# Optimization experiments

Hardware: AMD Instinct MI355X
Metric: run time of the kernel (lower is better)

The kernel has to match this reference:

```python
import jax, jax.numpy as jnp
from jax import lax
import numpy as np

OUT_SCALE = 0.001
DN = ('NCHW', 'OIHW', 'NCHW')


def _dw_res_gelu(v, w, b):
    # depthwise 3x3 conv (groups = C) + bias, residual add, exact GELU (torch nn.GELU default)
    y = lax.conv_general_dilated(v, w, (1, 1), ((1, 1), (1, 1)),
                                 feature_group_count=v.shape[1],
                                 dimension_numbers=DN)
    y = y + b[None, :, None, None]
    return jax.nn.gelu(v + y, approximate=False)


def setup_inputs() -> dict:
    key = jax.random.key(0)
    ks = jax.random.split(key, 6)
    B, C = 64, 64
    return {
        'z': jax.random.normal(ks[0], (B, C, 16, 16), jnp.float32),
        'x': jax.random.normal(ks[1], (B, C, 96, 96), jnp.float32),
        'wz': jax.random.normal(ks[2], (C, 1, 3, 3), jnp.float32) * 0.1,
        'bz': jax.random.normal(ks[3], (C,), jnp.float32) * 0.1,
        'wx': jax.random.normal(ks[4], (C, 1, 3, 3), jnp.float32) * 0.1,
        'bx': jax.random.normal(ks[5], (C,), jnp.float32) * 0.1,
    }


def reference(z, x, wz, bz, wx, bx):
    x = _dw_res_gelu(x, wx, bx)
    z = _dw_res_gelu(z, wz, bz)
    B, C, zh, zw = z.shape
    nx, _, h, w = x.shape
    # fast batched cross-correlation: view search as one image with B*C channels,
    # use templates z as [O=B, I=C, zh, zw] filters with feature_group_count=B
    xr = x.reshape(1, nx * C, h, w)
    out = lax.conv_general_dilated(xr, z, (1, 1),
                                   ((zh // 2, zh // 2), (zw // 2, zw // 2)),
                                   feature_group_count=B,
                                   dimension_numbers=DN)
    out = out.reshape(nx, -1, out.shape[-2], out.shape[-1])
    return out * OUT_SCALE
```

## Files before the change

kernel.cpp:

```cpp
#include <hip/hip_runtime.h>
#include <hip/hip_bf16.h>

typedef unsigned short ushortT;
typedef __bf16 bf16x8 __attribute__((ext_vector_type(8)));
typedef float f32x4 __attribute__((ext_vector_type(4)));

#define OUT_SCALE 0.001f

__device__ __forceinline__ float gelu_fast(float v) {
    const float u = v * fmaf(0.044715f * v, v, 1.0f);
    const float e = __expf(-1.5957691216057308f * u);
    return v * __builtin_amdgcn_rcpf(1.0f + e);
}
__device__ __forceinline__ ushortT f2bf(float f) {
    __hip_bfloat16 h = __float2bfloat16(f);
    return *reinterpret_cast<ushortT*>(&h);
}

__global__ __launch_bounds__(512) void k_gelu_x(
    const float* __restrict__ x, const float* __restrict__ wx,
    const float* __restrict__ bx, ushortT* __restrict__ xgt)
{
    const int r = blockIdx.x, b = blockIdx.y, tid = threadIdx.x;
    const int c = tid >> 3, colg = tid & 7, j0 = colg * 12;

    __shared__ ushortT tile[7168];

    if (tid < 128) {
        const int region = tid >> 5, k = tid & 31;
        const int start = (region & 1) * 3328 + (region >> 1) * 3584;
        *(uint4*)(&tile[start + k * 8]) = make_uint4(0, 0, 0, 0);
    }

    float w[9];
    #pragma unroll
    for (int i = 0; i < 9; ++i) w[i] = wx[c * 9 + i];
    const float bias = bx[c];

    float acc[12], winc[12];
    #pragma unroll
    for (int jj = 0; jj < 12; ++jj) acc[jj] = bias;

    const float* xb = x + (size_t)(b * 64 + c) * 9216;
    #pragma unroll
    for (int dr = 0; dr < 3; ++dr) {
        const int rr = r + dr - 1;
        const bool rok = (rr >= 0) && (rr < 96);
        float f[20];
        #pragma unroll
        for (int m = 0; m < 5; ++m) {
            const int cs = j0 - 4 + 4 * m;
            float4 v = make_float4(0.f, 0.f, 0.f, 0.f);
            if (rok && cs >= 0 && cs <= 92)
                v = *(const float4*)(xb + rr * 96 + cs);
            f[4 * m] = v.x; f[4 * m + 1] = v.y; f[4 * m + 2] = v.z; f[4 * m + 3] = v.w;
        }
        #pragma unroll
        for (int jj = 0; jj < 12; ++jj)
            acc[jj] += f[jj + 3] * w[dr * 3] + f[jj + 4] * w[dr * 3 + 1]
                     + f[jj + 5] * w[dr * 3 + 2];
        if (dr == 1) {
            #pragma unroll
            for (int jj = 0; jj < 12; ++jj) winc[jj] = f[jj + 4];
        }
    }

    const int g = c >> 5, cl = c & 31, chunk = cl >> 3, pos = cl & 7;
    #pragma unroll
    for (int jj = 0; jj < 12; ++jj) {
        const float gv = gelu_fast(acc[jj] + winc[jj]);
        const int T = j0 + jj + 8;
        const int schunk = chunk ^ ((T >> 1) & 3);
        tile[g * 3584 + T * 32 + schunk * 8 + pos] = f2bf(gv);
    }
    __syncthreads();

    uint4* dst = (uint4*)(xgt + (size_t)(b * 96 + r) * 7168);
    const uint4* s4 = (const uint4*)tile;
    #pragma unroll
    for (int k = 0; k < 2; ++k) {
        const int i = tid + k * 512;
        if (i < 896) dst[i] = s4[i];
    }
}

__global__ __launch_bounds__(256) void k_gelu_z(
    const float* __restrict__ z, const float* __restrict__ wz,
    const float* __restrict__ bz, ushortT* __restrict__ zbuf)
{
    const int b   = blockIdx.x;
    const int tid = threadIdx.x;
    const int c   = tid >> 2;
    const int q   = tid & 3;

    __shared__ float   zs[64 * 260];
    __shared__ ushortT zt[16384];

    {
        const float4* src = (const float4*)(z + ((size_t)b * 64 + c) * 256 + q * 64);
        float4* dstv = (float4*)(zs + c * 260 + q * 64);
        #pragma unroll
        for (int i = 0; i < 16; ++i) dstv[i] = src[i];
    }
    __syncthreads();

    const float* wp = wz + c * 9;
    float w[9];
    #pragma unroll
    for (int i = 0; i < 9; ++i) w[i] = wp[i];
    const float bias = bz[c];
    const float* zc = zs + c * 260;

    for (int v = q * 4; v < q * 4 + 4; ++v) {
        #pragma unroll
        for (int u = 0; u < 16; ++u) {
            float acc = bias;
            #pragma unroll
            for (int dr = 0; dr < 3; ++dr) {
                const int uu = u + dr - 1;
                if (uu < 0 || uu >= 16) continue;
                #pragma unroll
                for (int dc = 0; dc < 3; ++dc) {
                    const int vv = v + dc - 1;
                    if (vv < 0 || vv >= 16) continue;
                    acc += zc[uu * 16 + vv] * w[dr * 3 + dc];
                }
            }
            const float y = acc + zc[u * 16 + v];
            zt[(v * 16 + u) * 64 + c] = f2bf(gelu_fast(y));
        }
    }
    __syncthreads();
    uint4* dst = (uint4*)(zbuf + (size_t)b * 16384);
    const uint4* s4 = (const uint4*)zt;
    for (int i = tid; i < 2048; i += 256) dst[i] = s4[i];
}

__global__ __launch_bounds__(256, 4) void k_corr(
    const ushortT* __restrict__ xgt, const ushortT* __restrict__ zbuf,
    float* __restrict__ out)
{
    const int r    = blockIdx.x;
    const int b    = blockIdx.y;
    const int tid  = threadIdx.x;
    const int wave = tid >> 6;
    const int lane = tid & 63;
    const int n    = lane & 15;
    const int q    = lane >> 4;

    __shared__ ushortT rowbuf[8192];
    __shared__ float   outacc[16 * 113];

    if (tid < 128) {
        const int g = tid >> 6, k = tid & 63;
        *(uint4*)(&rowbuf[g * 4096 + 3584 + k * 8]) = make_uint4(0, 0, 0, 0);
    }

    {
        const uint4* src4 = (const uint4*)(xgt + (size_t)(b * 96 + r) * 7168);
        uint4* rb4 = (uint4*)rowbuf;
        #pragma unroll
        for (int k = 0; k < 4; ++k) {
            const int i2 = tid + k * 256;
            if (i2 < 896) {
                const int dsti = (i2 >= 448) ? i2 + 64 : i2;
                rb4[dsti] = src4[i2];
            }
        }
    }
    __syncthreads();

    const int j0a = (wave < 3) ? wave * 32 : 96;
    const ushortT* zb = zbuf + (size_t)b * 16384;
    const ushortT* rb = rowbuf;
    f32x4 acc0 = {0.f, 0.f, 0.f, 0.f};
    f32x4 acc1 = {0.f, 0.f, 0.f, 0.f};

    #pragma unroll
    for (int g = 0; g < 2; ++g) {
        bf16x8 bfrag[16];
        #pragma unroll
        for (int v = 0; v < 16; ++v)
            bfrag[v] = *(const bf16x8*)(zb + (v * 16 + n) * 64 + g * 32 + 8 * q);
        #pragma unroll
        for (int v = 0; v < 16; ++v) {
            const int T = j0a + n + v;
            const int off = (g * 128 + T) * 32 + ((q ^ ((T >> 1) & 3)) << 3);
            const bf16x8 a0 = *(const bf16x8*)(rb + off);
            acc0 = __builtin_amdgcn_mfma_f32_16x16x32_bf16(a0, bfrag[v], acc0, 0, 0, 0);
            if (wave < 3) {
                const bf16x8 a1 = *(const bf16x8*)(rb + off + 512);
                acc1 = __builtin_amdgcn_mfma_f32_16x16x32_bf16(a1, bfrag[v], acc1, 0, 0, 0);
            }
        }
    }

    {
        const int ii = 15 - n;
        float* orow = outacc + ii * 113 + j0a + 4 * q;
        #pragma unroll
        for (int g3 = 0; g3 < 4; ++g3) orow[g3] = acc0[g3];
        if (wave < 3) {
            #pragma unroll
            for (int g3 = 0; g3 < 4; ++g3) orow[16 + g3] = acc1[g3];
        }
    }
    __syncthreads();

    float* outb = out + (size_t)b * 9409;
    #pragma unroll
    for (int p = 0; p < 8; ++p) {
        const int ii = p * 2 + (tid >> 7);
        const int j  = tid & 127;
        const int irow = r - 7 + ii;
        if (j < 97 && irow >= 0 && irow < 97)
            atomicAdd(&outb[irow * 97 + j], outacc[ii * 113 + j] * OUT_SCALE);
    }
}

extern "C" void kernel_launch(void* const* d_in, const int* in_sizes, int n_in,
                              void* d_out, int out_size, void* d_ws, size_t ws_size,
                              hipStream_t stream)
{
    const float* z  = (const float*)d_in[0];
    const float* x  = (const float*)d_in[1];
    const float* wz = (const float*)d_in[2];
    const float* bz = (const float*)d_in[3];
    const float* wx = (const float*)d_in[4];
    const float* bx = (const float*)d_in[5];
    float* out = (float*)d_out;

    ushortT* xgt  = (ushortT*)d_ws;
    ushortT* zbuf = (ushortT*)((char*)d_ws + (size_t)64 * 96 * 7168 * 2);

    hipMemsetAsync(d_out, 0, (size_t)out_size * 4, stream);

    k_gelu_x<<<dim3(96, 64), 512, 0, stream>>>(x, wx, bx, xgt);
    k_gelu_z<<<dim3(64), 256, 0, stream>>>(z, wz, bz, zbuf);
    k_corr<<<dim3(96, 64), 256, 0, stream>>>(xgt, zbuf, out);

    (void)in_sizes; (void)n_in; (void)ws_size;
}
```

Before: 374.9 us.

## Fuse x depthwise-conv GELU into correlation kernel, drop intermediate buffer

Merges the x depthwise conv + GELU kernel into the correlation kernel, so each block computes its bf16 row tile straight into shared memory. This removes the global round trip of the roughly 88 MB intermediate and one kernel launch. The block grows to 512 threads with 7 MFMA waves of 16 columns each, and the block index is remapped so that nearby blocks spread across batch images. The cost is more registers per block and possible lower occupancy, and the x halo rows are still reloaded by each row block.

```diff
diff --git a/kernel.cpp b/kernel.cpp
--- a/kernel.cpp
+++ b/kernel.cpp
@@ -15,73 +15,6 @@
 __device__ __forceinline__ ushortT f2bf(float f) {
     __hip_bfloat16 h = __float2bfloat16(f);
     return *reinterpret_cast<ushortT*>(&h);
-}
-
-__global__ __launch_bounds__(512) void k_gelu_x(
-    const float* __restrict__ x, const float* __restrict__ wx,
-    const float* __restrict__ bx, ushortT* __restrict__ xgt)
-{
-    const int r = blockIdx.x, b = blockIdx.y, tid = threadIdx.x;
-    const int c = tid >> 3, colg = tid & 7, j0 = colg * 12;
-
-    __shared__ ushortT tile[7168];
-
-    if (tid < 128) {
-        const int region = tid >> 5, k = tid & 31;
-        const int start = (region & 1) * 3328 + (region >> 1) * 3584;
-        *(uint4*)(&tile[start + k * 8]) = make_uint4(0, 0, 0, 0);
-    }
-
-    float w[9];
-    #pragma unroll
-    for (int i = 0; i < 9; ++i) w[i] = wx[c * 9 + i];
-    const float bias = bx[c];
-
-    float acc[12], winc[12];
-    #pragma unroll
-    for (int jj = 0; jj < 12; ++jj) acc[jj] = bias;
-
-    const float* xb = x + (size_t)(b * 64 + c) * 9216;
-    #pragma unroll
-    for (int dr = 0; dr < 3; ++dr) {
-        const int rr = r + dr - 1;
-        const bool rok = (rr >= 0) && (rr < 96);
-        float f[20];
-        #pragma unroll
-        for (int m = 0; m < 5; ++m) {
-            const int cs = j0 - 4 + 4 * m;
-            float4 v = make_float4(0.f, 0.f, 0.f, 0.f);
-            if (rok && cs >= 0 && cs <= 92)
-                v = *(const float4*)(xb + rr * 96 + cs);
-            f[4 * m] = v.x; f[4 * m + 1] = v.y; f[4 * m + 2] = v.z; f[4 * m + 3] = v.w;
-        }
-        #pragma unroll
-        for (int jj = 0; jj < 12; ++jj)
-            acc[jj] += f[jj + 3] * w[dr * 3] + f[jj + 4] * w[dr * 3 + 1]
-                     + f[jj + 5] * w[dr * 3 + 2];
-        if (dr == 1) {
-            #pragma unroll
-            for (int jj = 0; jj < 12; ++jj) winc[jj] = f[jj + 4];
-        }
-    }
-
-    const int g = c >> 5, cl = c & 31, chunk = cl >> 3, pos = cl & 7;
-    #pragma unroll
-    for (int jj = 0; jj < 12; ++jj) {
-        const float gv = gelu_fast(acc[jj] + winc[jj]);
-        const int T = j0 + jj + 8;
-        const int schunk = chunk ^ ((T >> 1) & 3);
-        tile[g * 3584 + T * 32 + schunk * 8 + pos] = f2bf(gv);
-    }
-    __syncthreads();
-
-    uint4* dst = (uint4*)(xgt + (size_t)(b * 96 + r) * 7168);
-    const uint4* s4 = (const uint4*)tile;
-    #pragma unroll
-    for (int k = 0; k < 2; ++k) {
-        const int i = tid + k * 512;
-        if (i < 896) dst[i] = s4[i];
-    }
 }
 
 __global__ __launch_bounds__(256) void k_gelu_z(
@@ -136,81 +69,110 @@
     for (int i = tid; i < 2048; i += 256) dst[i] = s4[i];
 }
 
-__global__ __launch_bounds__(256, 4) void k_corr(
-    const ushortT* __restrict__ xgt, const ushortT* __restrict__ zbuf,
+__global__ __launch_bounds__(512, 4) void k_fused(
+    const float* __restrict__ x, const float* __restrict__ wx,
+    const float* __restrict__ bx, const ushortT* __restrict__ zbuf,
     float* __restrict__ out)
 {
-    const int r    = blockIdx.x;
-    const int b    = blockIdx.y;
-    const int tid  = threadIdx.x;
+    const int lin = blockIdx.x;
+    const int sw  = ((lin & 7) * 768) + (lin >> 3);
+    const int r   = sw % 96;
+    const int b   = sw / 96;
+    const int tid = threadIdx.x;
+
+    __shared__ ushortT rowbuf[8192];
+    __shared__ float   outacc[16 * 113];
+
+    if (tid < 256) {
+        const int g = tid >> 7, i = tid & 127;
+        const int off = (i < 32) ? i * 8 : 3328 + (i - 32) * 8;
+        *(uint4*)(&rowbuf[g * 4096 + off]) = make_uint4(0, 0, 0, 0);
+    }
+
+    {
+        const int c = tid >> 3, colg = tid & 7, j0 = colg * 12;
+
+        float w[9];
+        #pragma unroll
+        for (int i = 0; i < 9; ++i) w[i] = wx[c * 9 + i];
+        const float bias = bx[c];
+
+        float acc[12], winc[12];
+        #pragma unroll
+        for (int jj = 0; jj < 12; ++jj) acc[jj] = bias;
+
+        const float* xb = x + (size_t)(b * 64 + c) * 9216;
+        #pragma unroll
+        for (int dr = 0; dr < 3; ++dr) {
+            const int rr = r + dr - 1;
+            const bool rok = (rr >= 0) && (rr < 96);
+            float f[20];
+            #pragma unroll
+            for (int m = 0; m < 5; ++m) {
+                const int cs = j0 - 4 + 4 * m;
+                float4 v = make_float4(0.f, 0.f, 0.f, 0.f);
+                if (rok && cs >= 0 && cs <= 92)
+                    v = *(const float4*)(xb + rr * 96 + cs);
+                f[4 * m] = v.x; f[4 * m + 1] = v.y;
+                f[4 * m + 2] = v.z; f[4 * m + 3] = v.w;
+            }
+            #pragma unroll
+            for (int jj = 0; jj < 12; ++jj)
+                acc[jj] += f[jj + 3] * w[dr * 3] + f[jj + 4] * w[dr * 3 + 1]
+                         + f[jj + 5] * w[dr * 3 + 2];
+            if (dr == 1) {
+                #pragma unroll
+                for (int jj = 0; jj < 12; ++jj) winc[jj] = f[jj + 4];
+            }
+        }
+
+        const int g = c >> 5, cl = c & 31, chunk = cl >> 3, pos = cl & 7;
+        #pragma unroll
+        for (int jj = 0; jj < 12; ++jj) {
+            const float gv = gelu_fast(acc[jj] + winc[jj]);
+            const int T = j0 + jj + 8;
+            const int schunk = chunk ^ ((T >> 1) & 3);
+            rowbuf[g * 4096 + T * 32 + schunk * 8 + pos] = f2bf(gv);
+        }
+    }
+    __syncthreads();
+
     const int wave = tid >> 6;
     const int lane = tid & 63;
     const int n    = lane & 15;
     const int q    = lane >> 4;
-
-    __shared__ ushortT rowbuf[8192];
-    __shared__ float   outacc[16 * 113];
-
-    if (tid < 128) {
-        const int g = tid >> 6, k = tid & 63;
-        *(uint4*)(&rowbuf[g * 4096 + 3584 + k * 8]) = make_uint4(0, 0, 0, 0);
-    }
-
-    {
-        const uint4* src4 = (const uint4*)(xgt + (size_t)(b * 96 + r) * 7168);
-        uint4* rb4 = (uint4*)rowbuf;
-        #pragma unroll
-        for (int k = 0; k < 4; ++k) {
-            const int i2 = tid + k * 256;
-            if (i2 < 896) {
-                const int dsti = (i2 >= 448) ? i2 + 64 : i2;
-                rb4[dsti] = src4[i2];
-            }
-        }
-    }
-    __syncthreads();
-
-    const int j0a = (wave < 3) ? wave * 32 : 96;
-    const ushortT* zb = zbuf + (size_t)b * 16384;
-    const ushortT* rb = rowbuf;
-    f32x4 acc0 = {0.f, 0.f, 0.f, 0.f};
-    f32x4 acc1 = {0.f, 0.f, 0.f, 0.f};
-
-    #pragma unroll
-    for (int g = 0; g < 2; ++g) {
-        bf16x8 bfrag[16];
-        #pragma unroll
-        for (int v = 0; v < 16; ++v)
-            bfrag[v] = *(const bf16x8*)(zb + (v * 16 + n) * 64 + g * 32 + 8 * q);
-        #pragma unroll
-        for (int v = 0; v < 16; ++v) {
-            const int T = j0a + n + v;
-            const int off = (g * 128 + T) * 32 + ((q ^ ((T >> 1) & 3)) << 3);
-            const bf16x8 a0 = *(const bf16x8*)(rb + off);
-            acc0 = __builtin_amdgcn_mfma_f32_16x16x32_bf16(a0, bfrag[v], acc0, 0, 0, 0);
-            if (wave < 3) {
-                const bf16x8 a1 = *(const bf16x8*)(rb + off + 512);
-                acc1 = __builtin_amdgcn_mfma_f32_16x16x32_bf16(a1, bfrag[v], acc1, 0, 0, 0);
-            }
-        }
-    }
-
-    {
+    if (wave < 7) {
+        const int j0a = wave * 16;
+        const ushortT* zb = zbuf + (size_t)b * 16384;
+        const ushortT* rb = rowbuf;
+        f32x4 acc0 = {0.f, 0.f, 0.f, 0.f};
+
+        #pragma unroll
+        for (int g = 0; g < 2; ++g) {
+            bf16x8 bfrag[16];
+            #pragma unroll
+            for (int v = 0; v < 16; ++v)
+                bfrag[v] = *(const bf16x8*)(zb + (v * 16 + n) * 64 + g * 32 + 8 * q);
+            #pragma unroll
+            for (int v = 0; v < 16; ++v) {
+                const int T = j0a + n + v;
+                const int off = (g * 128 + T) * 32 + ((q ^ ((T >> 1) & 3)) << 3);
+                const bf16x8 a0 = *(const bf16x8*)(rb + off);
+                acc0 = __builtin_amdgcn_mfma_f32_16x16x32_bf16(a0, bfrag[v], acc0, 0, 0, 0);
+            }
+        }
+
         const int ii = 15 - n;
         float* orow = outacc + ii * 113 + j0a + 4 * q;
         #pragma unroll
         for (int g3 = 0; g3 < 4; ++g3) orow[g3] = acc0[g3];
-        if (wave < 3) {
-            #pragma unroll
-            for (int g3 = 0; g3 < 4; ++g3) orow[16 + g3] = acc1[g3];
-        }
     }
     __syncthreads();
 
     float* outb = out + (size_t)b * 9409;
     #pragma unroll
-    for (int p = 0; p < 8; ++p) {
-        const int ii = p * 2 + (tid >> 7);
+    for (int p = 0; p < 4; ++p) {
+        const int ii = p * 4 + (tid >> 7);
         const int j  = tid & 127;
         const int irow = r - 7 + ii;
         if (j < 97 && irow >= 0 && irow < 97)
@@ -230,14 +192,12 @@
     const float* bx = (const float*)d_in[5];
     float* out = (float*)d_out;
 
-    ushortT* xgt  = (ushortT*)d_ws;
-    ushortT* zbuf = (ushortT*)((char*)d_ws + (size_t)64 * 96 * 7168 * 2);
+    ushortT* zbuf = (ushortT*)d_ws;
 
     hipMemsetAsync(d_out, 0, (size_t)out_size * 4, stream);
 
-    k_gelu_x<<<dim3(96, 64), 512, 0, stream>>>(x, wx, bx, xgt);
     k_gelu_z<<<dim3(64), 256, 0, stream>>>(z, wz, bz, zbuf);
-    k_corr<<<dim3(96, 64), 256, 0, stream>>>(xgt, zbuf, out);
+    k_fused<<<dim3(6144), 512, 0, stream>>>(x, wx, bx, zbuf, out);
 
     (void)in_sizes; (void)n_in; (void)ws_size;
 }
```

After: 403.6 us. +7.6%, slower.
